# Optimization experiments

Measured on AMD Instinct MI355X. Metric: run time of the kernel, lower is better.

The kernel has to match this reference:

```python
import jax, jax.numpy as jnp
import numpy as np

N = 50000       # nodes
E = 800000      # edges
F_IN = 128      # num_node_features
H = 128         # hidden_channels
C = 10          # num_classes
G = 512         # graphs in batch


def _glorot(key, shape):
    fan_in, fan_out = shape
    lim = float(np.sqrt(6.0 / (fan_in + fan_out)))
    return jax.random.uniform(key, shape, jnp.float32, -lim, lim)


def setup_inputs() -> dict:
    key = jax.random.key(0)
    ks = jax.random.split(key, 12)
    x = jax.random.normal(ks[0], (N, F_IN), jnp.float32)
    edge_index = jax.random.randint(ks[1], (2, E), 0, N, dtype=jnp.int32).astype(jnp.int64)
    batch = jnp.sort(jax.random.randint(ks[2], (N,), 0, G, dtype=jnp.int32)).astype(jnp.int64)
    return {
        "x": x,
        "edge_index": edge_index,
        "batch": batch,
        "W1": _glorot(ks[3], (F_IN, H)), "b1": jnp.zeros((H,), jnp.float32),
        "W2": _glorot(ks[4], (H, H)),    "b2": jnp.zeros((H,), jnp.float32),
        "W3": _glorot(ks[5], (H, H)),    "b3": jnp.zeros((H,), jnp.float32),
        "W_lin": _glorot(ks[6], (H, C)), "b_lin": jnp.zeros((C,), jnp.float32),
    }


def _gcn_conv(h_in, W, b, src, dst, dis):
    # GCNConv: D^{-1/2} (A + I) D^{-1/2} (X W) + b  (symmetric norm, self-loops)
    h = h_in @ W                                   # [N, H]
    coef = (dis[src] * dis[dst])[:, None]          # [E, 1]
    msg = h[src] * coef                            # gather + scale
    agg = jax.ops.segment_sum(msg, dst, num_segments=N)  # scatter-add at targets
    agg = agg + h * (dis * dis)[:, None]           # self-loop term
    return agg + b


def reference(x, edge_index, batch, W1, b1, W2, b2, W3, b3, W_lin, b_lin):
    src, dst = edge_index[0], edge_index[1]
    # degree with self-loops (counted at aggregation target, PyG convention)
    deg = jax.ops.segment_sum(jnp.ones((E,), jnp.float32), dst, num_segments=N) + 1.0
    dis = jax.lax.rsqrt(deg)

    h = jax.nn.relu(_gcn_conv(x, W1, b1, src, dst, dis))
    h = jax.nn.relu(_gcn_conv(h, W2, b2, src, dst, dis))
    h = _gcn_conv(h, W3, b3, src, dst, dis)

    # global mean pool over graphs
    counts = jax.ops.segment_sum(jnp.ones((N,), jnp.float32), batch, num_segments=G)
    pooled = jax.ops.segment_sum(h, batch, num_segments=G)
    pooled = pooled / jnp.maximum(counts, 1.0)[:, None]

    # dropout(p=0.5, training=False) -> identity
    return pooled @ W_lin + b_lin
```

## Files before the change

### kernel.cpp

```cpp
#include <hip/hip_runtime.h>

#define NN 50000
#define NE 800000
#define FD 128
#define NG 512
#define NC 10

#define NBUCK 98
#define BSHIFT 9
#define BSTRIDE 10240
#define P1_EPB 4096
#define P1_BLOCKS ((NE + P1_EPB - 1) / P1_EPB)

typedef __attribute__((ext_vector_type(8))) short bf16x8;
typedef __attribute__((ext_vector_type(4))) float f32x4;


__device__ __forceinline__ float bf2f(unsigned short u) {
  return __uint_as_float(((unsigned int)u) << 16);
}
__device__ __forceinline__ unsigned short f2bf(float f) {
  unsigned int b = __float_as_uint(f);
  b += 0x7FFF + ((b >> 16) & 1);
  return (unsigned short)(b >> 16);
}
__device__ __forceinline__ float blo(unsigned int u) {
  return __uint_as_float(u << 16);
}
__device__ __forceinline__ float bhi(unsigned int u) {
  return __uint_as_float(u & 0xFFFF0000u);
}


__global__ __launch_bounds__(128) void init_kernel(int* __restrict__ gcursor) {
  int i = threadIdx.x;
  if (i < NBUCK) gcursor[i] = i * BSTRIDE;
}

__global__ __launch_bounds__(1024) void pass1_kernel(const int* __restrict__ ei,
                                                     int* __restrict__ gcursor,
                                                     unsigned int* __restrict__ bucketBuf) {
  __shared__ int bh[NBUCK];
  __shared__ int gbase[NBUCK];
  __shared__ int bcur[NBUCK];

  int tid = threadIdx.x;
  int e0 = blockIdx.x * P1_EPB;
  int ne = NE - e0; if (ne > P1_EPB) ne = P1_EPB;

  if (tid < NBUCK) bh[tid] = 0;
  __syncthreads();

  for (int i = tid; i < ne; i += 1024) {
    int d = ei[NE + e0 + i];
    atomicAdd(&bh[d >> BSHIFT], 1);
  }
  __syncthreads();

  if (tid < NBUCK) {
    bcur[tid] = 0;
    gbase[tid] = (bh[tid] > 0) ? atomicAdd(&gcursor[tid], bh[tid]) : 0;
  }
  __syncthreads();

  for (int i = tid; i < ne; i += 1024) {
    int s = ei[e0 + i];
    int d = ei[NE + e0 + i];
    int b = d >> BSHIFT;
    int p = atomicAdd(&bcur[b], 1);
    bucketBuf[gbase[b] + p] = (unsigned int)s | ((unsigned int)d << 16);
  }
}

__global__ __launch_bounds__(128) void bucket_scan_kernel(const int* __restrict__ gcur,
                                                          int* __restrict__ bbase) {
  __shared__ int s[128];
  int tid = threadIdx.x;
  int c = (tid < NBUCK) ? (gcur[tid] - tid * BSTRIDE) : 0;
  s[tid] = c;
  __syncthreads();
  for (int off = 1; off < 128; off <<= 1) {
    int v = (tid >= off) ? s[tid - off] : 0;
    __syncthreads();
    s[tid] += v;
    __syncthreads();
  }
  if (tid < NBUCK) bbase[tid] = s[tid] - c;
}

__global__ __launch_bounds__(1024) void pass2_kernel(const unsigned int* __restrict__ bucketBuf,
                                                     const int* __restrict__ gcur,
                                                     const int* __restrict__ bbase,
                                                     int* __restrict__ offs,
                                                     float* __restrict__ dis,
                                                     unsigned short* __restrict__ csr) {
  __shared__ unsigned int raw[BSTRIDE];
  __shared__ unsigned short sorted[BSTRIDE];
  __shared__ int h[512], pos[512], cur[512];

  int b = blockIdx.x;
  int tid = threadIdx.x;
  int nStart = b << BSHIFT;
  int cnt = gcur[b] - b * BSTRIDE;
  if (cnt > BSTRIDE) cnt = BSTRIDE;
  int eStart = bbase[b];

  for (int i = tid; i < cnt; i += 1024) raw[i] = bucketBuf[(size_t)b * BSTRIDE + i];
  if (tid < 512) h[tid] = 0;
  __syncthreads();

  for (int i = tid; i < cnt; i += 1024) atomicAdd(&h[(raw[i] >> 16) - nStart], 1);
  __syncthreads();

  if (tid < 512) pos[tid] = h[tid];
  __syncthreads();
  #pragma unroll
  for (int off = 1; off < 512; off <<= 1) {
    int v = 0;
    if (tid < 512 && tid >= off) v = pos[tid - off];
    __syncthreads();
    if (tid < 512) pos[tid] += v;
    __syncthreads();
  }
  if (tid < 512) {
    int ex = pos[tid] - h[tid];
    cur[tid] = ex;
    int n = nStart + tid;
    if (n < NN) {
      offs[n] = eStart + ex;
      dis[n] = rsqrtf((float)h[tid] + 1.0f);
    }
  }
  if (b == NBUCK - 1 && tid == 0) offs[NN] = eStart + cnt;
  __syncthreads();

  for (int i = tid; i < cnt; i += 1024) {
    unsigned int r = raw[i];
    int d = (int)(r >> 16) - nStart;
    int p = atomicAdd(&cur[d], 1);
    sorted[p] = (unsigned short)(r & 0xFFFFu);
  }
  __syncthreads();

  for (int i = tid; i < cnt; i += 1024) csr[eStart + i] = sorted[i];
}


__global__ __launch_bounds__(256) void prep_w_kernel(const float* __restrict__ W,
                                                     unsigned short* __restrict__ wf) {
  int i = blockIdx.x * 256 + threadIdx.x;
  if (i >= 16384) return;
  int j = i & 7, l = (i >> 3) & 63, ks = (i >> 9) & 3, ct = i >> 11;
  int k = ks * 32 + (l >> 4) * 8 + j;
  int c = ct * 16 + (l & 15);
  float w = W[k * 128 + c];
  unsigned int bb = __float_as_uint(w);
  unsigned int bh = bb & 0xFFFF0000u;
  float r = w - __uint_as_float(bh);
  int base = (((ct * 4 + ks) * 2 + 0) * 64 + l) * 8 + j;
  wf[base] = (unsigned short)(bh >> 16);
  wf[base + 512] = f2bf(r);
}


__global__ __launch_bounds__(256) void gemm_mfma_kernel(const float* __restrict__ A,
                                                        const unsigned short* __restrict__ wf,
                                                        unsigned short* __restrict__ Hb,
                                                        int applyRelu) {
  __shared__ unsigned short ldsW[32768];
  int tid = threadIdx.x;
  {
    const uint4* src = reinterpret_cast<const uint4*>(wf);
    uint4* dst = reinterpret_cast<uint4*>(ldsW);
    #pragma unroll
    for (int i = 0; i < 16; ++i) dst[tid + i * 256] = src[tid + i * 256];
  }
  __syncthreads();

  int w = tid >> 6, lane = tid & 63;
  int rowbase = blockIdx.x * 128 + w * 32;
  int kgrp = lane >> 4;
  int r0 = rowbase + (lane & 15);
  int r1 = r0 + 16;
  int a0 = (r0 < NN) ? r0 : 0;
  int a1 = (r1 < NN) ? r1 : 0;

  f32x4 acc0[8], acc1[8];
  #pragma unroll
  for (int ct = 0; ct < 8; ++ct) {
    f32x4 z = {0.f, 0.f, 0.f, 0.f};
    acc0[ct] = z; acc1[ct] = z;
  }

  #pragma unroll
  for (int ks = 0; ks < 4; ++ks) {
    bf16x8 ahi0, alo0, ahi1, alo1;
    {
      const float* ap = A + (size_t)a0 * FD + ks * 32 + kgrp * 8;
      float4 v0 = *reinterpret_cast<const float4*>(ap);
      float4 v1 = *reinterpret_cast<const float4*>(ap + 4);
      float a[8] = {v0.x, v0.y, v0.z, v0.w, v1.x, v1.y, v1.z, v1.w};
      #pragma unroll
      for (int j = 0; j < 8; ++j) {
        float v = a[j];
        if (applyRelu) v = fmaxf(v, 0.f);
        unsigned int bb = __float_as_uint(v);
        unsigned int bh = bb & 0xFFFF0000u;
        float r = v - __uint_as_float(bh);
        ahi0[j] = (short)(bh >> 16);
        alo0[j] = (short)f2bf(r);
      }
    }
    {
      const float* ap = A + (size_t)a1 * FD + ks * 32 + kgrp * 8;
      float4 v0 = *reinterpret_cast<const float4*>(ap);
      float4 v1 = *reinterpret_cast<const float4*>(ap + 4);
      float a[8] = {v0.x, v0.y, v0.z, v0.w, v1.x, v1.y, v1.z, v1.w};
      #pragma unroll
      for (int j = 0; j < 8; ++j) {
        float v = a[j];
        if (applyRelu) v = fmaxf(v, 0.f);
        unsigned int bb = __float_as_uint(v);
        unsigned int bh = bb & 0xFFFF0000u;
        float r = v - __uint_as_float(bh);
        ahi1[j] = (short)(bh >> 16);
        alo1[j] = (short)f2bf(r);
      }
    }
    #pragma unroll
    for (int ct = 0; ct < 8; ++ct) {
      int off = (((ct * 4 + ks) * 2) * 64 + lane) * 8;
      bf16x8 bhiV = *reinterpret_cast<const bf16x8*>(&ldsW[off]);
      bf16x8 bloV = *reinterpret_cast<const bf16x8*>(&ldsW[off + 512]);
      acc0[ct] = __builtin_amdgcn_mfma_f32_16x16x32_bf16(ahi0, bhiV, acc0[ct], 0, 0, 0);
      acc1[ct] = __builtin_amdgcn_mfma_f32_16x16x32_bf16(ahi1, bhiV, acc1[ct], 0, 0, 0);
      acc0[ct] = __builtin_amdgcn_mfma_f32_16x16x32_bf16(alo0, bhiV, acc0[ct], 0, 0, 0);
      acc1[ct] = __builtin_amdgcn_mfma_f32_16x16x32_bf16(alo1, bhiV, acc1[ct], 0, 0, 0);
      acc0[ct] = __builtin_amdgcn_mfma_f32_16x16x32_bf16(ahi0, bloV, acc0[ct], 0, 0, 0);
      acc1[ct] = __builtin_amdgcn_mfma_f32_16x16x32_bf16(ahi1, bloV, acc1[ct], 0, 0, 0);
    }
  }

  int ccol = lane & 15;
  #pragma unroll
  for (int g = 0; g < 2; ++g) {
    int crow0 = rowbase + g * 16 + kgrp * 4;
    #pragma unroll
    for (int i = 0; i < 4; ++i) {
      int r = crow0 + i;
      if (r < NN) {
        #pragma unroll
        for (int ct = 0; ct < 8; ++ct) {
          float v = g ? acc1[ct][i] : acc0[ct][i];
          Hb[(size_t)r * FD + ct * 16 + ccol] = f2bf(v);
        }
      }
    }
  }
}


__global__ __launch_bounds__(256) void agg_edge_kernel(const int* __restrict__ offs,
                                                       const unsigned short* __restrict__ csr,
                                                       const float* __restrict__ dis,
                                                       const unsigned short* __restrict__ Hb,
                                                       const float* __restrict__ b,
                                                       float* __restrict__ AGG) {
  int node = blockIdx.x * 4 + (threadIdx.x >> 6);
  if (node >= NN) return;
  node = __builtin_amdgcn_readfirstlane(node);
  int lane = threadIdx.x & 63;
  int q = lane >> 4;
  int ch = (lane & 15) * 8;
  int beg = offs[node], end = offs[node + 1];
  float disn = dis[node];

  float accP[8], accQ[8];
  #pragma unroll
  for (int k = 0; k < 8; ++k) { accP[k] = 0.f; accQ[k] = 0.f; }

  if (q == 0) {
    float d2 = disn * disn;
    float4 b0 = *reinterpret_cast<const float4*>(&b[ch]);
    float4 b1 = *reinterpret_cast<const float4*>(&b[ch + 4]);
    uint4 hn = *reinterpret_cast<const uint4*>(&Hb[(size_t)node * FD + ch]);
    accP[0] = b0.x + d2 * blo(hn.x); accP[1] = b0.y + d2 * bhi(hn.x);
    accP[2] = b0.z + d2 * blo(hn.y); accP[3] = b0.w + d2 * bhi(hn.y);
    accP[4] = b1.x + d2 * blo(hn.z); accP[5] = b1.y + d2 * bhi(hn.z);
    accP[6] = b1.z + d2 * blo(hn.w); accP[7] = b1.w + d2 * bhi(hn.w);
  }

  int last = end - 1;
  for (int j = beg; j < end; j += 16) {
    int e0 = j + q, e1 = j + q + 4, e2 = j + q + 8, e3 = j + q + 12;
    int i0 = (e0 <= last) ? e0 : last;
    int i1 = (e1 <= last) ? e1 : last;
    int i2 = (e2 <= last) ? e2 : last;
    int i3 = (e3 <= last) ? e3 : last;
    int s0 = csr[i0], s1 = csr[i1], s2 = csr[i2], s3 = csr[i3];
    float c0 = (e0 <= last) ? dis[s0] * disn : 0.f;
    float c1 = (e1 <= last) ? dis[s1] * disn : 0.f;
    float c2 = (e2 <= last) ? dis[s2] * disn : 0.f;
    float c3 = (e3 <= last) ? dis[s3] * disn : 0.f;
    uint4 h0 = *reinterpret_cast<const uint4*>(&Hb[(size_t)s0 * FD + ch]);
    uint4 h1 = *reinterpret_cast<const uint4*>(&Hb[(size_t)s1 * FD + ch]);
    uint4 h2 = *reinterpret_cast<const uint4*>(&Hb[(size_t)s2 * FD + ch]);
    uint4 h3 = *reinterpret_cast<const uint4*>(&Hb[(size_t)s3 * FD + ch]);
    accP[0] += c0 * blo(h0.x); accP[1] += c0 * bhi(h0.x);
    accP[2] += c0 * blo(h0.y); accP[3] += c0 * bhi(h0.y);
    accP[4] += c0 * blo(h0.z); accP[5] += c0 * bhi(h0.z);
    accP[6] += c0 * blo(h0.w); accP[7] += c0 * bhi(h0.w);
    accQ[0] += c1 * blo(h1.x); accQ[1] += c1 * bhi(h1.x);
    accQ[2] += c1 * blo(h1.y); accQ[3] += c1 * bhi(h1.y);
    accQ[4] += c1 * blo(h1.z); accQ[5] += c1 * bhi(h1.z);
    accQ[6] += c1 * blo(h1.w); accQ[7] += c1 * bhi(h1.w);
    accP[0] += c2 * blo(h2.x); accP[1] += c2 * bhi(h2.x);
    accP[2] += c2 * blo(h2.y); accP[3] += c2 * bhi(h2.y);
    accP[4] += c2 * blo(h2.z); accP[5] += c2 * bhi(h2.z);
    accP[6] += c2 * blo(h2.w); accP[7] += c2 * bhi(h2.w);
    accQ[0] += c3 * blo(h3.x); accQ[1] += c3 * bhi(h3.x);
    accQ[2] += c3 * blo(h3.y); accQ[3] += c3 * bhi(h3.y);
    accQ[4] += c3 * blo(h3.z); accQ[5] += c3 * bhi(h3.z);
    accQ[6] += c3 * blo(h3.w); accQ[7] += c3 * bhi(h3.w);
  }

  #pragma unroll
  for (int k = 0; k < 8; ++k) {
    float v = accP[k] + accQ[k];
    v += __shfl_xor(v, 16, 64);
    v += __shfl_xor(v, 32, 64);
    accP[k] = v;
  }

  if (q == 0) {
    float4 o0 = make_float4(accP[0], accP[1], accP[2], accP[3]);
    float4 o1 = make_float4(accP[4], accP[5], accP[6], accP[7]);
    *reinterpret_cast<float4*>(&AGG[(size_t)node * FD + ch]) = o0;
    *reinterpret_cast<float4*>(&AGG[(size_t)node * FD + ch + 4]) = o1;
  }
}


__device__ __forceinline__ int lower_bound(const int* __restrict__ b, int n, int key) {
  int lo = 0, hi = n;
  while (lo < hi) {
    int m = (lo + hi) >> 1;
    if (b[m] < key) lo = m + 1; else hi = m;
  }
  return lo;
}

__global__ __launch_bounds__(256) void pool_final_kernel(const float* __restrict__ AGG,
                                                         const int* __restrict__ batch,
                                                         const float* __restrict__ Wl,
                                                         const float* __restrict__ bl,
                                                         float* __restrict__ out) {
  int g = blockIdx.x;
  int tid = threadIdx.x;
  int lane = tid & 63, w = tid >> 6;
  int start = lower_bound(batch, NN, g);
  int end = lower_bound(batch, NN, g + 1);

  const float2* AGG2 = reinterpret_cast<const float2*>(AGG);
  float2 acc = make_float2(0.f, 0.f);
  for (int n = start + w; n < end; n += 4) {
    float2 v = AGG2[(size_t)n * 64 + lane];
    acc.x += v.x; acc.y += v.y;
  }
  __shared__ float red[4][FD];
  red[w][lane * 2 + 0] = acc.x;
  red[w][lane * 2 + 1] = acc.y;
  __syncthreads();
  if (w == 0) {
    float px = red[0][lane * 2] + red[1][lane * 2] + red[2][lane * 2] + red[3][lane * 2];
    float py = red[0][lane * 2 + 1] + red[1][lane * 2 + 1] + red[2][lane * 2 + 1] + red[3][lane * 2 + 1];
    float inv = 1.0f / fmaxf((float)(end - start), 1.0f);
    px *= inv; py *= inv;
    float pc[NC];
    #pragma unroll
    for (int c = 0; c < NC; ++c)
      pc[c] = px * Wl[(2 * lane) * NC + c] + py * Wl[(2 * lane + 1) * NC + c];
    #pragma unroll
    for (int off = 32; off > 0; off >>= 1) {
      #pragma unroll
      for (int c = 0; c < NC; ++c) pc[c] += __shfl_down(pc[c], off, 64);
    }
    if (lane == 0) {
      #pragma unroll
      for (int c = 0; c < NC; ++c) out[g * NC + c] = pc[c] + bl[c];
    }
  }
}


extern "C" void kernel_launch(void* const* d_in, const int* in_sizes, int n_in,
                              void* d_out, int out_size, void* d_ws, size_t ws_size,
                              hipStream_t stream) {
  const float* x       = (const float*)d_in[0];
  const int* ei        = (const int*)d_in[1];
  const int* batch     = (const int*)d_in[2];
  const float* W1 = (const float*)d_in[3];
  const float* b1 = (const float*)d_in[4];
  const float* W2 = (const float*)d_in[5];
  const float* b2 = (const float*)d_in[6];
  const float* W3 = (const float*)d_in[7];
  const float* b3 = (const float*)d_in[8];
  const float* Wl = (const float*)d_in[9];
  const float* bl = (const float*)d_in[10];
  float* out = (float*)d_out;

  char* ws = (char*)d_ws;
  size_t o = 0;
  auto alloc = [&](size_t bytes) {
    void* p = ws + o;
    o += bytes;
    o = (o + 255) & ~(size_t)255;
    return p;
  };
  int*   offs   = (int*)  alloc((size_t)(NN + 1) * 4);
  float* dis    = (float*)alloc((size_t)NN * 4);
  int*   gcur   = (int*)  alloc((size_t)NBUCK * 4);
  int*   bbase  = (int*)  alloc((size_t)NBUCK * 4);
  unsigned int* bucketBuf = (unsigned int*)alloc((size_t)NBUCK * BSTRIDE * 4);
  unsigned short* csr = (unsigned short*)alloc((size_t)NE * 2);
  unsigned short* hb  = (unsigned short*)alloc((size_t)NN * FD * 2);
  float* agg    = (float*)alloc((size_t)NN * FD * 4);
  unsigned short* wf1 = (unsigned short*)alloc((size_t)2 * FD * FD * 2);
  unsigned short* wf2 = (unsigned short*)alloc((size_t)2 * FD * FD * 2);
  unsigned short* wf3 = (unsigned short*)alloc((size_t)2 * FD * FD * 2);

  init_kernel<<<1, 128, 0, stream>>>(gcur);
  pass1_kernel<<<P1_BLOCKS, 1024, 0, stream>>>(ei, gcur, bucketBuf);
  bucket_scan_kernel<<<1, 128, 0, stream>>>(gcur, bbase);
  pass2_kernel<<<NBUCK, 1024, 0, stream>>>(bucketBuf, gcur, bbase, offs, dis, csr);
  prep_w_kernel<<<64, 256, 0, stream>>>(W1, wf1);
  prep_w_kernel<<<64, 256, 0, stream>>>(W2, wf2);
  prep_w_kernel<<<64, 256, 0, stream>>>(W3, wf3);

  int gemmGrid = (NN + 127) / 128;
  int nodeGrid = (NN + 3) / 4;

  gemm_mfma_kernel<<<gemmGrid, 256, 0, stream>>>(x, wf1, hb, 0);
  agg_edge_kernel<<<nodeGrid, 256, 0, stream>>>(offs, csr, dis, hb, b1, agg);
  gemm_mfma_kernel<<<gemmGrid, 256, 0, stream>>>(agg, wf2, hb, 1);
  agg_edge_kernel<<<nodeGrid, 256, 0, stream>>>(offs, csr, dis, hb, b2, agg);
  gemm_mfma_kernel<<<gemmGrid, 256, 0, stream>>>(agg, wf3, hb, 1);
  agg_edge_kernel<<<nodeGrid, 256, 0, stream>>>(offs, csr, dis, hb, b3, agg);

  pool_final_kernel<<<NG, 256, 0, stream>>>(agg, batch, Wl, bl, out);
}
```

Before: 197.3 us.

## Store intermediate activations in bf16 and fold source normalization into GEMM output

The GEMM epilogue now multiplies each row by dis[src], so the edge aggregation only sums pre-scaled rows and applies dis[dst] and the bias once at the end, which removes the per-edge dis gather. Layers 1 and 2 write their aggregated output as bf16, and the following GEMMs read bf16 activations with ReLU applied by sign check. This halves activation read/write traffic and drops the hi/lo split MFMA passes on the A operand. The cost is lower precision, since activations are rounded to bf16 and pre-scaled values are rounded before aggregation.

```diff
diff --git a/kernel.cpp b/kernel.cpp
--- a/kernel.cpp
+++ b/kernel.cpp
@@ -16,9 +16,6 @@
 typedef __attribute__((ext_vector_type(4))) float f32x4;
 
 
-__device__ __forceinline__ float bf2f(unsigned short u) {
-  return __uint_as_float(((unsigned int)u) << 16);
-}
 __device__ __forceinline__ unsigned short f2bf(float f) {
   unsigned int b = __float_as_uint(f);
   b += 0x7FFF + ((b >> 16) & 1);
@@ -163,10 +160,10 @@
 }
 
 
-__global__ __launch_bounds__(256) void gemm_mfma_kernel(const float* __restrict__ A,
-                                                        const unsigned short* __restrict__ wf,
-                                                        unsigned short* __restrict__ Hb,
-                                                        int applyRelu) {
+__global__ __launch_bounds__(256) void gemm_f32_kernel(const float* __restrict__ A,
+                                                       const unsigned short* __restrict__ wf,
+                                                       const float* __restrict__ dis,
+                                                       unsigned short* __restrict__ Hs) {
   __shared__ unsigned short ldsW[32768];
   int tid = threadIdx.x;
   {
@@ -202,11 +199,9 @@
       float a[8] = {v0.x, v0.y, v0.z, v0.w, v1.x, v1.y, v1.z, v1.w};
       #pragma unroll
       for (int j = 0; j < 8; ++j) {
-        float v = a[j];
-        if (applyRelu) v = fmaxf(v, 0.f);
-        unsigned int bb = __float_as_uint(v);
+        unsigned int bb = __float_as_uint(a[j]);
         unsigned int bh = bb & 0xFFFF0000u;
-        float r = v - __uint_as_float(bh);
+        float r = a[j] - __uint_as_float(bh);
         ahi0[j] = (short)(bh >> 16);
         alo0[j] = (short)f2bf(r);
       }
@@ -218,11 +213,9 @@
       float a[8] = {v0.x, v0.y, v0.z, v0.w, v1.x, v1.y, v1.z, v1.w};
       #pragma unroll
       for (int j = 0; j < 8; ++j) {
-        float v = a[j];
-        if (applyRelu) v = fmaxf(v, 0.f);
-        unsigned int bb = __float_as_uint(v);
+        unsigned int bb = __float_as_uint(a[j]);
         unsigned int bh = bb & 0xFFFF0000u;
-        float r = v - __uint_as_float(bh);
+        float r = a[j] - __uint_as_float(bh);
         ahi1[j] = (short)(bh >> 16);
         alo1[j] = (short)f2bf(r);
       }
@@ -249,10 +242,11 @@
     for (int i = 0; i < 4; ++i) {
       int r = crow0 + i;
       if (r < NN) {
+        float dv = dis[r];
         #pragma unroll
         for (int ct = 0; ct < 8; ++ct) {
           float v = g ? acc1[ct][i] : acc0[ct][i];
-          Hb[(size_t)r * FD + ct * 16 + ccol] = f2bf(v);
+          Hs[(size_t)r * FD + ct * 16 + ccol] = f2bf(dv * v);
         }
       }
     }
@@ -260,12 +254,99 @@
 }
 
 
+__global__ __launch_bounds__(256) void gemm_bf16_kernel(const unsigned short* __restrict__ Ab,
+                                                        const unsigned short* __restrict__ wf,
+                                                        const float* __restrict__ dis,
+                                                        unsigned short* __restrict__ Hs) {
+  __shared__ unsigned short ldsW[32768];
+  int tid = threadIdx.x;
+  {
+    const uint4* src = reinterpret_cast<const uint4*>(wf);
+    uint4* dst = reinterpret_cast<uint4*>(ldsW);
+    #pragma unroll
+    for (int i = 0; i < 16; ++i) dst[tid + i * 256] = src[tid + i * 256];
+  }
+  __syncthreads();
+
+  int w = tid >> 6, lane = tid & 63;
+  int rowbase = blockIdx.x * 128 + w * 32;
+  int kgrp = lane >> 4;
+  int r0 = rowbase + (lane & 15);
+  int r1 = r0 + 16;
+  int a0 = (r0 < NN) ? r0 : 0;
+  int a1 = (r1 < NN) ? r1 : 0;
+
+  f32x4 acc0[8], acc1[8];
+  #pragma unroll
+  for (int ct = 0; ct < 8; ++ct) {
+    f32x4 z = {0.f, 0.f, 0.f, 0.f};
+    acc0[ct] = z; acc1[ct] = z;
+  }
+
+  #pragma unroll
+  for (int ks = 0; ks < 4; ++ks) {
+    bf16x8 av0, av1;
+    {
+      uint4 u = *reinterpret_cast<const uint4*>(&Ab[(size_t)a0 * FD + ks * 32 + kgrp * 8]);
+      unsigned int uu[4] = {u.x, u.y, u.z, u.w};
+      #pragma unroll
+      for (int p = 0; p < 4; ++p) {
+        unsigned short lo16 = (unsigned short)(uu[p] & 0xFFFFu);
+        unsigned short hi16 = (unsigned short)(uu[p] >> 16);
+        av0[2 * p + 0] = (short)(((short)lo16 < 0) ? 0 : lo16);
+        av0[2 * p + 1] = (short)(((short)hi16 < 0) ? 0 : hi16);
+      }
+    }
+    {
+      uint4 u = *reinterpret_cast<const uint4*>(&Ab[(size_t)a1 * FD + ks * 32 + kgrp * 8]);
+      unsigned int uu[4] = {u.x, u.y, u.z, u.w};
+      #pragma unroll
+      for (int p = 0; p < 4; ++p) {
+        unsigned short lo16 = (unsigned short)(uu[p] & 0xFFFFu);
+        unsigned short hi16 = (unsigned short)(uu[p] >> 16);
+        av1[2 * p + 0] = (short)(((short)lo16 < 0) ? 0 : lo16);
+        av1[2 * p + 1] = (short)(((short)hi16 < 0) ? 0 : hi16);
+      }
+    }
+    #pragma unroll
+    for (int ct = 0; ct < 8; ++ct) {
+      int off = (((ct * 4 + ks) * 2) * 64 + lane) * 8;
+      bf16x8 bhiV = *reinterpret_cast<const bf16x8*>(&ldsW[off]);
+      bf16x8 bloV = *reinterpret_cast<const bf16x8*>(&ldsW[off + 512]);
+      acc0[ct] = __builtin_amdgcn_mfma_f32_16x16x32_bf16(av0, bhiV, acc0[ct], 0, 0, 0);
+      acc1[ct] = __builtin_amdgcn_mfma_f32_16x16x32_bf16(av1, bhiV, acc1[ct], 0, 0, 0);
+      acc0[ct] = __builtin_amdgcn_mfma_f32_16x16x32_bf16(av0, bloV, acc0[ct], 0, 0, 0);
+      acc1[ct] = __builtin_amdgcn_mfma_f32_16x16x32_bf16(av1, bloV, acc1[ct], 0, 0, 0);
+    }
+  }
+
+  int ccol = lane & 15;
+  #pragma unroll
+  for (int g = 0; g < 2; ++g) {
+    int crow0 = rowbase + g * 16 + kgrp * 4;
+    #pragma unroll
+    for (int i = 0; i < 4; ++i) {
+      int r = crow0 + i;
+      if (r < NN) {
+        float dv = dis[r];
+        #pragma unroll
+        for (int ct = 0; ct < 8; ++ct) {
+          float v = g ? acc1[ct][i] : acc0[ct][i];
+          Hs[(size_t)r * FD + ct * 16 + ccol] = f2bf(dv * v);
+        }
+      }
+    }
+  }
+}
+
+
+template <bool OUT32>
 __global__ __launch_bounds__(256) void agg_edge_kernel(const int* __restrict__ offs,
                                                        const unsigned short* __restrict__ csr,
                                                        const float* __restrict__ dis,
-                                                       const unsigned short* __restrict__ Hb,
-                                                       const float* __restrict__ b,
-                                                       float* __restrict__ AGG) {
+                                                       const unsigned short* __restrict__ Hs,
+                                                       const float* __restrict__ bias,
+                                                       void* __restrict__ AGG) {
   int node = blockIdx.x * 4 + (threadIdx.x >> 6);
   if (node >= NN) return;
   node = __builtin_amdgcn_readfirstlane(node);
@@ -280,14 +361,11 @@
   for (int k = 0; k < 8; ++k) { accP[k] = 0.f; accQ[k] = 0.f; }
 
   if (q == 0) {
-    float d2 = disn * disn;
-    float4 b0 = *reinterpret_cast<const float4*>(&b[ch]);
-    float4 b1 = *reinterpret_cast<const float4*>(&b[ch + 4]);
-    uint4 hn = *reinterpret_cast<const uint4*>(&Hb[(size_t)node * FD + ch]);
-    accP[0] = b0.x + d2 * blo(hn.x); accP[1] = b0.y + d2 * bhi(hn.x);
-    accP[2] = b0.z + d2 * blo(hn.y); accP[3] = b0.w + d2 * bhi(hn.y);
-    accP[4] = b1.x + d2 * blo(hn.z); accP[5] = b1.y + d2 * bhi(hn.z);
-    accP[6] = b1.z + d2 * blo(hn.w); accP[7] = b1.w + d2 * bhi(hn.w);
+    uint4 hn = *reinterpret_cast<const uint4*>(&Hs[(size_t)node * FD + ch]);
+    accP[0] = blo(hn.x); accP[1] = bhi(hn.x);
+    accP[2] = blo(hn.y); accP[3] = bhi(hn.y);
+    accP[4] = blo(hn.z); accP[5] = bhi(hn.z);
+    accP[6] = blo(hn.w); accP[7] = bhi(hn.w);
   }
 
   int last = end - 1;
@@ -297,46 +375,63 @@
     int i1 = (e1 <= last) ? e1 : last;
     int i2 = (e2 <= last) ? e2 : last;
     int i3 = (e3 <= last) ? e3 : last;
+    float m0 = (e0 <= last) ? 1.f : 0.f;
+    float m1 = (e1 <= last) ? 1.f : 0.f;
+    float m2 = (e2 <= last) ? 1.f : 0.f;
+    float m3 = (e3 <= last) ? 1.f : 0.f;
     int s0 = csr[i0], s1 = csr[i1], s2 = csr[i2], s3 = csr[i3];
-    float c0 = (e0 <= last) ? dis[s0] * disn : 0.f;
-    float c1 = (e1 <= last) ? dis[s1] * disn : 0.f;
-    float c2 = (e2 <= last) ? dis[s2] * disn : 0.f;
-    float c3 = (e3 <= last) ? dis[s3] * disn : 0.f;
-    uint4 h0 = *reinterpret_cast<const uint4*>(&Hb[(size_t)s0 * FD + ch]);
-    uint4 h1 = *reinterpret_cast<const uint4*>(&Hb[(size_t)s1 * FD + ch]);
-    uint4 h2 = *reinterpret_cast<const uint4*>(&Hb[(size_t)s2 * FD + ch]);
-    uint4 h3 = *reinterpret_cast<const uint4*>(&Hb[(size_t)s3 * FD + ch]);
-    accP[0] += c0 * blo(h0.x); accP[1] += c0 * bhi(h0.x);
-    accP[2] += c0 * blo(h0.y); accP[3] += c0 * bhi(h0.y);
-    accP[4] += c0 * blo(h0.z); accP[5] += c0 * bhi(h0.z);
-    accP[6] += c0 * blo(h0.w); accP[7] += c0 * bhi(h0.w);
-    accQ[0] += c1 * blo(h1.x); accQ[1] += c1 * bhi(h1.x);
-    accQ[2] += c1 * blo(h1.y); accQ[3] += c1 * bhi(h1.y);
-    accQ[4] += c1 * blo(h1.z); accQ[5] += c1 * bhi(h1.z);
-    accQ[6] += c1 * blo(h1.w); accQ[7] += c1 * bhi(h1.w);
-    accP[0] += c2 * blo(h2.x); accP[1] += c2 * bhi(h2.x);
-    accP[2] += c2 * blo(h2.y); accP[3] += c2 * bhi(h2.y);
-    accP[4] += c2 * blo(h2.z); accP[5] += c2 * bhi(h2.z);
-    accP[6] += c2 * blo(h2.w); accP[7] += c2 * bhi(h2.w);
-    accQ[0] += c3 * blo(h3.x); accQ[1] += c3 * bhi(h3.x);
-    accQ[2] += c3 * blo(h3.y); accQ[3] += c3 * bhi(h3.y);
-    accQ[4] += c3 * blo(h3.z); accQ[5] += c3 * bhi(h3.z);
-    accQ[6] += c3 * blo(h3.w); accQ[7] += c3 * bhi(h3.w);
-  }
-
+    uint4 h0 = *reinterpret_cast<const uint4*>(&Hs[(size_t)s0 * FD + ch]);
+    uint4 h1 = *reinterpret_cast<const uint4*>(&Hs[(size_t)s1 * FD + ch]);
+    uint4 h2 = *reinterpret_cast<const uint4*>(&Hs[(size_t)s2 * FD + ch]);
+    uint4 h3 = *reinterpret_cast<const uint4*>(&Hs[(size_t)s3 * FD + ch]);
+    accP[0] += m0 * blo(h0.x); accP[1] += m0 * bhi(h0.x);
+    accP[2] += m0 * blo(h0.y); accP[3] += m0 * bhi(h0.y);
+    accP[4] += m0 * blo(h0.z); accP[5] += m0 * bhi(h0.z);
+    accP[6] += m0 * blo(h0.w); accP[7] += m0 * bhi(h0.w);
+    accQ[0] += m1 * blo(h1.x); accQ[1] += m1 * bhi(h1.x);
+    accQ[2] += m1 * blo(h1.y); accQ[3] += m1 * bhi(h1.y);
+    accQ[4] += m1 * blo(h1.z); accQ[5] += m1 * bhi(h1.z);
+    accQ[6] += m1 * blo(h1.w); accQ[7] += m1 * bhi(h1.w);
+    accP[0] += m2 * blo(h2.x); accP[1] += m2 * bhi(h2.x);
+    accP[2] += m2 * blo(h2.y); accP[3] += m2 * bhi(h2.y);
+    accP[4] += m2 * blo(h2.z); accP[5] += m2 * bhi(h2.z);
+    accP[6] += m2 * blo(h2.w); accP[7] += m2 * bhi(h2.w);
+    accQ[0] += m3 * blo(h3.x); accQ[1] += m3 * bhi(h3.x);
+    accQ[2] += m3 * blo(h3.y); accQ[3] += m3 * bhi(h3.y);
+    accQ[4] += m3 * blo(h3.z); accQ[5] += m3 * bhi(h3.z);
+    accQ[6] += m3 * blo(h3.w); accQ[7] += m3 * bhi(h3.w);
+  }
+
+  float outv[8];
   #pragma unroll
   for (int k = 0; k < 8; ++k) {
     float v = accP[k] + accQ[k];
     v += __shfl_xor(v, 16, 64);
     v += __shfl_xor(v, 32, 64);
-    accP[k] = v;
+    outv[k] = v;
   }
 
   if (q == 0) {
-    float4 o0 = make_float4(accP[0], accP[1], accP[2], accP[3]);
-    float4 o1 = make_float4(accP[4], accP[5], accP[6], accP[7]);
-    *reinterpret_cast<float4*>(&AGG[(size_t)node * FD + ch]) = o0;
-    *reinterpret_cast<float4*>(&AGG[(size_t)node * FD + ch + 4]) = o1;
+    float4 b0 = *reinterpret_cast<const float4*>(&bias[ch]);
+    float4 b1 = *reinterpret_cast<const float4*>(&bias[ch + 4]);
+    float o[8];
+    o[0] = b0.x + disn * outv[0]; o[1] = b0.y + disn * outv[1];
+    o[2] = b0.z + disn * outv[2]; o[3] = b0.w + disn * outv[3];
+    o[4] = b1.x + disn * outv[4]; o[5] = b1.y + disn * outv[5];
+    o[6] = b1.z + disn * outv[6]; o[7] = b1.w + disn * outv[7];
+    if (OUT32) {
+      float* dst = reinterpret_cast<float*>(AGG) + (size_t)node * FD + ch;
+      *reinterpret_cast<float4*>(dst) = make_float4(o[0], o[1], o[2], o[3]);
+      *reinterpret_cast<float4*>(dst + 4) = make_float4(o[4], o[5], o[6], o[7]);
+    } else {
+      uint4 pk;
+      pk.x = (unsigned int)f2bf(o[0]) | ((unsigned int)f2bf(o[1]) << 16);
+      pk.y = (unsigned int)f2bf(o[2]) | ((unsigned int)f2bf(o[3]) << 16);
+      pk.z = (unsigned int)f2bf(o[4]) | ((unsigned int)f2bf(o[5]) << 16);
+      pk.w = (unsigned int)f2bf(o[6]) | ((unsigned int)f2bf(o[7]) << 16);
+      unsigned short* dst = reinterpret_cast<unsigned short*>(AGG) + (size_t)node * FD + ch;
+      *reinterpret_cast<uint4*>(dst) = pk;
+    }
   }
 }
 
@@ -422,9 +517,10 @@
   int*   gcur   = (int*)  alloc((size_t)NBUCK * 4);
   int*   bbase  = (int*)  alloc((size_t)NBUCK * 4);
   unsigned int* bucketBuf = (unsigned int*)alloc((size_t)NBUCK * BSTRIDE * 4);
-  unsigned short* csr = (unsigned short*)alloc((size_t)NE * 2);
-  unsigned short* hb  = (unsigned short*)alloc((size_t)NN * FD * 2);
-  float* agg    = (float*)alloc((size_t)NN * FD * 4);
+  unsigned short* csr  = (unsigned short*)alloc((size_t)NE * 2);
+  unsigned short* hs   = (unsigned short*)alloc((size_t)NN * FD * 2);
+  unsigned short* aggb = (unsigned short*)alloc((size_t)NN * FD * 2);
+  float* aggf   = (float*)alloc((size_t)NN * FD * 4);
   unsigned short* wf1 = (unsigned short*)alloc((size_t)2 * FD * FD * 2);
   unsigned short* wf2 = (unsigned short*)alloc((size_t)2 * FD * FD * 2);
   unsigned short* wf3 = (unsigned short*)alloc((size_t)2 * FD * FD * 2);
@@ -440,12 +536,12 @@
   int gemmGrid = (NN + 127) / 128;
   int nodeGrid = (NN + 3) / 4;
 
-  gemm_mfma_kernel<<<gemmGrid, 256, 0, stream>>>(x, wf1, hb, 0);
-  agg_edge_kernel<<<nodeGrid, 256, 0, stream>>>(offs, csr, dis, hb, b1, agg);
-  gemm_mfma_kernel<<<gemmGrid, 256, 0, stream>>>(agg, wf2, hb, 1);
-  agg_edge_kernel<<<nodeGrid, 256, 0, stream>>>(offs, csr, dis, hb, b2, agg);
-  gemm_mfma_kernel<<<gemmGrid, 256, 0, stream>>>(agg, wf3, hb, 1);
-  agg_edge_kernel<<<nodeGrid, 256, 0, stream>>>(offs, csr, dis, hb, b3, agg);
-
-  pool_final_kernel<<<NG, 256, 0, stream>>>(agg, batch, Wl, bl, out);
-}
+  gemm_f32_kernel<<<gemmGrid, 256, 0, stream>>>(x, wf1, dis, hs);
+  agg_edge_kernel<false><<<nodeGrid, 256, 0, stream>>>(offs, csr, dis, hs, b1, aggb);
+  gemm_bf16_kernel<<<gemmGrid, 256, 0, stream>>>(aggb, wf2, dis, hs);
+  agg_edge_kernel<false><<<nodeGrid, 256, 0, stream>>>(offs, csr, dis, hs, b2, aggb);
+  gemm_bf16_kernel<<<gemmGrid, 256, 0, stream>>>(aggb, wf3, dis, hs);
+  agg_edge_kernel<true><<<nodeGrid, 256, 0, stream>>>(offs, csr, dis, hs, b3, aggf);
+
+  pool_final_kernel<<<NG, 256, 0, stream>>>(aggf, batch, Wl, bl, out);
+}
```

Result: faster. 180.6 us (-8.5%).
